# Performance work log

Hardware: AMD Instinct MI355X
Metric: run time of the kernel (lower is better)

The kernel has to match this reference:

```python
import jax, jax.numpy as jnp
import numpy as np

BETA = 1.0

def setup_inputs() -> dict:
    key = jax.random.key(0)
    k1, k2 = jax.random.split(key)
    g = jax.random.normal(k1, (4, 2048, 4096), dtype=jnp.float32)
    W = jax.random.normal(k2, (4096, 16384), dtype=jnp.float32) * 0.02
    return {"g": g, "W": W}

def reference(g, W):
    # column-normalize W over the input dim n (dim=0 in torch)
    norm = jnp.linalg.norm(W, axis=0, keepdims=True)  # [1, n_hidden]
    hidsig = jnp.einsum('btn,nh->bth', g, W / norm)    # [B, T, n_hidden]
    hidlag = (1.0 / BETA) * jax.nn.logsumexp(BETA * hidsig, axis=-1)  # [B, T]
    return hidlag.reshape(-1, hidlag.shape[-1])
```

## Files before the change

kernel.cpp:

```cpp
#include <hip/hip_runtime.h>
#include <hip/hip_bf16.h>

#define M_TOTAL 8192
#define K_DIM   4096
#define H_DIM   16384

#define BM 256
#define BN 256
#define BK 64
#define NKT (K_DIM / BK)

typedef __attribute__((ext_vector_type(8))) short   short8;
typedef __attribute__((ext_vector_type(4))) float   f32x4;
typedef __attribute__((ext_vector_type(8))) unsigned short u16x8;

static __device__ __forceinline__ unsigned short f2bf(float f) {
    unsigned int x = __float_as_uint(f);
    x += 0x7fffu + ((x >> 16) & 1u);
    return (unsigned short)(x >> 16);
}

__global__ void cast_bf16_kernel(const float* __restrict__ in,
                                 unsigned short* __restrict__ out, long n) {
    long i = ((long)blockIdx.x * blockDim.x + threadIdx.x) * 8;
    if (i >= n) return;
    const float4* p = (const float4*)(in + i);
    float4 a = p[0];
    float4 b = p[1];
    u16x8 o;
    o[0] = f2bf(a.x); o[1] = f2bf(a.y); o[2] = f2bf(a.z); o[3] = f2bf(a.w);
    o[4] = f2bf(b.x); o[5] = f2bf(b.y); o[6] = f2bf(b.z); o[7] = f2bf(b.w);
    *(u16x8*)(out + i) = o;
}

__global__ void transpose_norm_kernel(const float* __restrict__ W,
                                      unsigned short* __restrict__ Wt,
                                      float* __restrict__ norm2) {
    __shared__ float tile[64][65];
    __shared__ float np[64];
    const int h0 = blockIdx.x * 64;
    const int n0 = blockIdx.y * 64;
    const int t  = threadIdx.x;
    const int c  = t & 63;
    const int r4 = t >> 6;

    if (t < 64) np[t] = 0.f;
    __syncthreads();

    float sq = 0.f;
#pragma unroll
    for (int it = 0; it < 16; ++it) {
        int r = it * 4 + r4;
        float v = W[(size_t)(n0 + r) * H_DIM + h0 + c];
        tile[r][c] = v;
        sq += v * v;
    }
    atomicAdd(&np[c], sq);
    __syncthreads();

    const int chunk = t & 7;
    const int hr    = t >> 3;
#pragma unroll
    for (int it = 0; it < 2; ++it) {
        int hrow = hr + it * 32;
        u16x8 o;
#pragma unroll
        for (int j = 0; j < 8; ++j)
            o[j] = f2bf(tile[chunk * 8 + j][hrow]);
        *(u16x8*)&Wt[(size_t)(h0 + hrow) * K_DIM + n0 + chunk * 8] = o;
    }
    if (t < 64) atomicAdd(&norm2[h0 + t], np[t]);
}

__global__ __launch_bounds__(512, 2)
void gemm_lse_kernel(const unsigned short* __restrict__ A,
                     const unsigned short* __restrict__ Bt,
                     const float* __restrict__ norm2,
                     float* __restrict__ sums) {
    __shared__ __attribute__((aligned(16))) unsigned short As[2][BM][BK];
    __shared__ __attribute__((aligned(16))) unsigned short Bs[2][BN][BK];

    const int tid  = threadIdx.x;
    const int wave = tid >> 6;
    const int lane = tid & 63;
    const int l15  = lane & 15;
    const int quad = lane >> 4;
    const int wm   = wave >> 2;
    const int wn   = wave & 3;

    const int bid = blockIdx.x;
    const int xcd = bid & 7;
    const int li  = bid >> 3;
    const int m0  = ((xcd & 1) * 16 + (li & 15)) * BM;
    const int h0  = ((xcd >> 1) * 16 + (li >> 4)) * BN;

    const int ri = lane >> 3;
    const int sc = ((lane & 7) ^ ri) * 8;
    const unsigned short* ag = A  + (size_t)(m0 + wave * 8 + ri) * K_DIM + sc;
    const unsigned short* bg = Bt + (size_t)(h0 + wave * 8 + ri) * K_DIM + sc;

#define STAGE_A(BF_, BASE_, KT_)                                               \
    __builtin_amdgcn_global_load_lds(                                          \
        (const __attribute__((address_space(1))) void*)                        \
            (ag + (size_t)(BASE_) * K_DIM + (KT_) * BK),                       \
        (__attribute__((address_space(3))) void*)&As[BF_][(BASE_) + wave * 8][0], \
        16, 0, 0)
#define STAGE_B(BF_, BASE_, KT_)                                               \
    __builtin_amdgcn_global_load_lds(                                          \
        (const __attribute__((address_space(1))) void*)                        \
            (bg + (size_t)(BASE_) * K_DIM + (KT_) * BK),                       \
        (__attribute__((address_space(3))) void*)&Bs[BF_][(BASE_) + wave * 8][0], \
        16, 0, 0)

    const int arow = wm * 128 + l15;
    const int brow = wn * 64 + l15;
    const int sl0  = ((quad)     ^ (l15 & 7)) * 8;
    const int sl1  = ((4 + quad) ^ (l15 & 7)) * 8;

#define LDA(D_, BF_, FM_, KS_) D_ = *(const short8*)&As[BF_][arow + (FM_) * 16][(KS_) ? sl1 : sl0]
#define LDB(D_, BF_, FN_, KS_) D_ = *(const short8*)&Bs[BF_][brow + (FN_) * 16][(KS_) ? sl1 : sl0]

    f32x4 acc[8][4];
#pragma unroll
    for (int i = 0; i < 8; ++i)
#pragma unroll
        for (int j = 0; j < 4; ++j)
            acc[i][j] = (f32x4){0.f, 0.f, 0.f, 0.f};

    short8 sa0[4], sb0[4], sa1[4], sb1[4];

#define CLUSTER(FB_, SA_, SB_)                                                 \
    __builtin_amdgcn_s_barrier();                                              \
    __builtin_amdgcn_s_setprio(1);                                             \
    _Pragma("unroll")                                                          \
    for (int fm = 0; fm < 4; ++fm)                                             \
        _Pragma("unroll")                                                      \
        for (int fn = 0; fn < 4; ++fn)                                         \
            acc[(FB_) + fm][fn] = __builtin_amdgcn_mfma_f32_16x16x32_bf16(     \
                SA_[fm], SB_[fn], acc[(FB_) + fm][fn], 0, 0, 0);               \
    __builtin_amdgcn_s_setprio(0);                                             \
    __builtin_amdgcn_s_barrier()

    STAGE_A(0, 0, 0);   STAGE_A(0, 128, 0);
    STAGE_A(0, 64, 0);  STAGE_A(0, 192, 0);
    STAGE_B(0, 0, 0);   STAGE_B(0, 64, 0);
    STAGE_B(0, 128, 0); STAGE_B(0, 192, 0);
    STAGE_A(1, 0, 1);   STAGE_A(1, 128, 1);
    STAGE_B(1, 0, 1);   STAGE_B(1, 64, 1);
    STAGE_B(1, 128, 1); STAGE_B(1, 192, 1);
    asm volatile("s_waitcnt vmcnt(6)" ::: "memory");
    __builtin_amdgcn_s_barrier();

    LDA(sa0[0], 0, 0, 0); LDA(sa0[1], 0, 1, 0);
    LDA(sa0[2], 0, 2, 0); LDA(sa0[3], 0, 3, 0);
    LDB(sb0[0], 0, 0, 0); LDB(sb0[1], 0, 1, 0);
    LDB(sb0[2], 0, 2, 0); LDB(sb0[3], 0, 3, 0);

#pragma unroll 2
    for (int t = 0; t < NKT; ++t) {
        const int buf  = t & 1;
        const int nbuf = buf ^ 1;

        LDA(sa1[0], buf, 0, 1); LDA(sa1[1], buf, 1, 1);
        LDA(sa1[2], buf, 2, 1); LDA(sa1[3], buf, 3, 1);
        LDB(sb1[0], buf, 0, 1); LDB(sb1[1], buf, 1, 1);
        LDB(sb1[2], buf, 2, 1); LDB(sb1[3], buf, 3, 1);
        if (t < NKT - 1) { STAGE_A(nbuf, 64, t + 1); STAGE_A(nbuf, 192, t + 1); }
        asm volatile("s_waitcnt vmcnt(8)" ::: "memory");
        CLUSTER(0, sa0, sb0);

        LDA(sa0[0], buf, 4, 0); LDA(sa0[1], buf, 5, 0);
        LDA(sa0[2], buf, 6, 0); LDA(sa0[3], buf, 7, 0);
        CLUSTER(0, sa1, sb1);

        LDA(sa1[0], buf, 4, 1); LDA(sa1[1], buf, 5, 1);
        LDA(sa1[2], buf, 6, 1); LDA(sa1[3], buf, 7, 1);
        if (t < NKT - 2) { STAGE_A(buf, 0, t + 2); STAGE_A(buf, 128, t + 2); }
        asm volatile("s_waitcnt vmcnt(4)" ::: "memory");
        CLUSTER(4, sa0, sb0);

        if (t < NKT - 1) {
            LDA(sa0[0], nbuf, 0, 0); LDA(sa0[1], nbuf, 1, 0);
            LDA(sa0[2], nbuf, 2, 0); LDA(sa0[3], nbuf, 3, 0);
            LDB(sb0[0], nbuf, 0, 0); LDB(sb0[1], nbuf, 1, 0);
            LDB(sb0[2], nbuf, 2, 0); LDB(sb0[3], nbuf, 3, 0);
        }
        if (t < NKT - 2) {
            STAGE_B(buf, 0, t + 2);   STAGE_B(buf, 64, t + 2);
            STAGE_B(buf, 128, t + 2); STAGE_B(buf, 192, t + 2);
        }
        CLUSTER(4, sa1, sb1);
    }

    float rn[4];
#pragma unroll
    for (int fn = 0; fn < 4; ++fn)
        rn[fn] = rsqrtf(norm2[h0 + wn * 64 + fn * 16 + l15]);

#pragma unroll
    for (int fm = 0; fm < 8; ++fm) {
#pragma unroll
        for (int r2 = 0; r2 < 4; ++r2) {
            float s = 0.f;
#pragma unroll
            for (int fn = 0; fn < 4; ++fn)
                s += __expf(acc[fm][fn][r2] * rn[fn]);
            s += __shfl_xor(s, 1);
            s += __shfl_xor(s, 2);
            s += __shfl_xor(s, 4);
            s += __shfl_xor(s, 8);
            if (l15 == 0)
                atomicAdd(&sums[m0 + wm * 128 + fm * 16 + quad * 4 + r2], s);
        }
    }
#undef STAGE_A
#undef STAGE_B
#undef LDA
#undef LDB
#undef CLUSTER
}

__global__ void finalize_kernel(const float* __restrict__ sums,
                                float* __restrict__ out, int n) {
    int i = blockIdx.x * blockDim.x + threadIdx.x;
    if (i < n) out[i] = logf(sums[i]);
}

extern "C" void kernel_launch(void* const* d_in, const int* in_sizes, int n_in,
                              void* d_out, int out_size, void* d_ws, size_t ws_size,
                              hipStream_t stream) {
    const float* g = (const float*)d_in[0];
    const float* W = (const float*)d_in[1];
    float* out = (float*)d_out;

    char* ws = (char*)d_ws;
    unsigned short* gbf   = (unsigned short*)ws;
    unsigned short* wt    = (unsigned short*)(ws + (size_t)67108864);
    float*          norm2 = (float*)(ws + (size_t)67108864 + 134217728);
    float*          sums  = (float*)(ws + (size_t)67108864 + 134217728 + 65536);

    hipMemsetAsync(norm2, 0, (H_DIM + M_TOTAL) * sizeof(float), stream);

    cast_bf16_kernel<<<(M_TOTAL * (long)K_DIM) / (256 * 8), 256, 0, stream>>>(
        g, gbf, (long)M_TOTAL * K_DIM);

    transpose_norm_kernel<<<dim3(H_DIM / 64, K_DIM / 64), 256, 0, stream>>>(
        W, wt, norm2);

    gemm_lse_kernel<<<(H_DIM / BN) * (M_TOTAL / BM), 512, 0, stream>>>(
        gbf, wt, norm2, sums);

    finalize_kernel<<<(M_TOTAL + 255) / 256, 256, 0, stream>>>(sums, out, M_TOTAL);
}
```

Before: 1.352 ms.

## Restructure GEMM main loop into two MFMA clusters with single-stage prefetch

Rewrites the K-loop schedule from four interleaved MFMA clusters with partial vmcnt waits and two-tile-ahead global prefetch into two clusters (low and high A halves). Each cluster covers both k-subslices and ends with a full vmcnt(0) wait. Global staging now runs only one tile ahead, and A/B fragment register sets are reorganised to hold both k-steps. This simplifies the dependency tracking and issues larger MFMA bursts, but it shortens the prefetch distance and forces full memory drains each half-iteration, so global load latency may be less hidden.

```diff
diff --git a/kernel.cpp b/kernel.cpp
--- a/kernel.cpp
+++ b/kernel.cpp
@@ -127,69 +127,65 @@
         for (int j = 0; j < 4; ++j)
             acc[i][j] = (f32x4){0.f, 0.f, 0.f, 0.f};
 
-    short8 sa0[4], sb0[4], sa1[4], sb1[4];
-
-#define CLUSTER(FB_, SA_, SB_)                                                 \
+    short8 aL[4][2], aH[4][2], b[4][2];
+
+#define CLUSTER(SA_, FB_)                                                      \
     __builtin_amdgcn_s_barrier();                                              \
     __builtin_amdgcn_s_setprio(1);                                             \
     _Pragma("unroll")                                                          \
-    for (int fm = 0; fm < 4; ++fm)                                             \
+    for (int ks = 0; ks < 2; ++ks)                                             \
         _Pragma("unroll")                                                      \
-        for (int fn = 0; fn < 4; ++fn)                                         \
-            acc[(FB_) + fm][fn] = __builtin_amdgcn_mfma_f32_16x16x32_bf16(     \
-                SA_[fm], SB_[fn], acc[(FB_) + fm][fn], 0, 0, 0);               \
+        for (int fm = 0; fm < 4; ++fm)                                         \
+            _Pragma("unroll")                                                  \
+            for (int fn = 0; fn < 4; ++fn)                                     \
+                acc[(FB_) + fm][fn] = __builtin_amdgcn_mfma_f32_16x16x32_bf16( \
+                    SA_[fm][ks], b[fn][ks], acc[(FB_) + fm][fn], 0, 0, 0);     \
     __builtin_amdgcn_s_setprio(0);                                             \
+    asm volatile("s_waitcnt vmcnt(0)" ::: "memory");                           \
     __builtin_amdgcn_s_barrier()
 
-    STAGE_A(0, 0, 0);   STAGE_A(0, 128, 0);
-    STAGE_A(0, 64, 0);  STAGE_A(0, 192, 0);
+    STAGE_A(0, 0, 0);   STAGE_A(0, 64, 0);
+    STAGE_A(0, 128, 0); STAGE_A(0, 192, 0);
     STAGE_B(0, 0, 0);   STAGE_B(0, 64, 0);
     STAGE_B(0, 128, 0); STAGE_B(0, 192, 0);
-    STAGE_A(1, 0, 1);   STAGE_A(1, 128, 1);
-    STAGE_B(1, 0, 1);   STAGE_B(1, 64, 1);
-    STAGE_B(1, 128, 1); STAGE_B(1, 192, 1);
-    asm volatile("s_waitcnt vmcnt(6)" ::: "memory");
+    asm volatile("s_waitcnt vmcnt(0)" ::: "memory");
     __builtin_amdgcn_s_barrier();
 
-    LDA(sa0[0], 0, 0, 0); LDA(sa0[1], 0, 1, 0);
-    LDA(sa0[2], 0, 2, 0); LDA(sa0[3], 0, 3, 0);
-    LDB(sb0[0], 0, 0, 0); LDB(sb0[1], 0, 1, 0);
-    LDB(sb0[2], 0, 2, 0); LDB(sb0[3], 0, 3, 0);
+    LDA(aL[0][0], 0, 0, 0); LDA(aL[1][0], 0, 1, 0);
+    LDA(aL[2][0], 0, 2, 0); LDA(aL[3][0], 0, 3, 0);
+    LDA(aL[0][1], 0, 0, 1); LDA(aL[1][1], 0, 1, 1);
+    LDA(aL[2][1], 0, 2, 1); LDA(aL[3][1], 0, 3, 1);
 
 #pragma unroll 2
     for (int t = 0; t < NKT; ++t) {
         const int buf  = t & 1;
         const int nbuf = buf ^ 1;
 
-        LDA(sa1[0], buf, 0, 1); LDA(sa1[1], buf, 1, 1);
-        LDA(sa1[2], buf, 2, 1); LDA(sa1[3], buf, 3, 1);
-        LDB(sb1[0], buf, 0, 1); LDB(sb1[1], buf, 1, 1);
-        LDB(sb1[2], buf, 2, 1); LDB(sb1[3], buf, 3, 1);
-        if (t < NKT - 1) { STAGE_A(nbuf, 64, t + 1); STAGE_A(nbuf, 192, t + 1); }
-        asm volatile("s_waitcnt vmcnt(8)" ::: "memory");
-        CLUSTER(0, sa0, sb0);
-
-        LDA(sa0[0], buf, 4, 0); LDA(sa0[1], buf, 5, 0);
-        LDA(sa0[2], buf, 6, 0); LDA(sa0[3], buf, 7, 0);
-        CLUSTER(0, sa1, sb1);
-
-        LDA(sa1[0], buf, 4, 1); LDA(sa1[1], buf, 5, 1);
-        LDA(sa1[2], buf, 6, 1); LDA(sa1[3], buf, 7, 1);
-        if (t < NKT - 2) { STAGE_A(buf, 0, t + 2); STAGE_A(buf, 128, t + 2); }
-        asm volatile("s_waitcnt vmcnt(4)" ::: "memory");
-        CLUSTER(4, sa0, sb0);
-
         if (t < NKT - 1) {
-            LDA(sa0[0], nbuf, 0, 0); LDA(sa0[1], nbuf, 1, 0);
-            LDA(sa0[2], nbuf, 2, 0); LDA(sa0[3], nbuf, 3, 0);
-            LDB(sb0[0], nbuf, 0, 0); LDB(sb0[1], nbuf, 1, 0);
-            LDB(sb0[2], nbuf, 2, 0); LDB(sb0[3], nbuf, 3, 0);
+            STAGE_A(nbuf, 0, t + 1);   STAGE_A(nbuf, 64, t + 1);
+            STAGE_A(nbuf, 128, t + 1); STAGE_A(nbuf, 192, t + 1);
         }
-        if (t < NKT - 2) {
-            STAGE_B(buf, 0, t + 2);   STAGE_B(buf, 64, t + 2);
-            STAGE_B(buf, 128, t + 2); STAGE_B(buf, 192, t + 2);
+        LDB(b[0][0], buf, 0, 0); LDB(b[1][0], buf, 1, 0);
+        LDB(b[2][0], buf, 2, 0); LDB(b[3][0], buf, 3, 0);
+        LDB(b[0][1], buf, 0, 1); LDB(b[1][1], buf, 1, 1);
+        LDB(b[2][1], buf, 2, 1); LDB(b[3][1], buf, 3, 1);
+        LDA(aH[0][0], buf, 4, 0); LDA(aH[1][0], buf, 5, 0);
+        LDA(aH[2][0], buf, 6, 0); LDA(aH[3][0], buf, 7, 0);
+        LDA(aH[0][1], buf, 4, 1); LDA(aH[1][1], buf, 5, 1);
+        LDA(aH[2][1], buf, 6, 1); LDA(aH[3][1], buf, 7, 1);
+
+        CLUSTER(aL, 0);
+
+        if (t < NKT - 1) {
+            STAGE_B(nbuf, 0, t + 1);   STAGE_B(nbuf, 64, t + 1);
+            STAGE_B(nbuf, 128, t + 1); STAGE_B(nbuf, 192, t + 1);
+            LDA(aL[0][0], nbuf, 0, 0); LDA(aL[1][0], nbuf, 1, 0);
+            LDA(aL[2][0], nbuf, 2, 0); LDA(aL[3][0], nbuf, 3, 0);
+            LDA(aL[0][1], nbuf, 0, 1); LDA(aL[1][1], nbuf, 1, 1);
+            LDA(aL[2][1], nbuf, 2, 1); LDA(aL[3][1], nbuf, 3, 1);
         }
-        CLUSTER(4, sa1, sb1);
+
+        CLUSTER(aH, 4);
     }
 
     float rn[4];
```

Result: slower. 1.560 ms (+15.4%).

## Reschedule GEMM main loop with one barrier per MFMA cluster and earlier staging

Applied to the files above, without the earlier changes.

Restructures the double-buffered bf16 MFMA main loop so each of the four MFMA clusters is preceded by a single barrier plus a priority raise, instead of a barrier before and after every cluster. Global-to-LDS stage loads are issued right after the barrier, ahead of the LDS fragment reads, and the vmcnt waits move to the loop top and before the B staging, with separate counts for the last iterations. The goal is to halve the barrier count and overlap global loads with MFMA work better. The new wait counts must still guard every LDS buffer reuse, and a miscount could create a race.

```diff
diff --git a/kernel.cpp b/kernel.cpp
--- a/kernel.cpp
+++ b/kernel.cpp
@@ -129,17 +129,13 @@
 
     short8 sa0[4], sb0[4], sa1[4], sb1[4];
 
-#define CLUSTER(FB_, SA_, SB_)                                                 \
-    __builtin_amdgcn_s_barrier();                                              \
-    __builtin_amdgcn_s_setprio(1);                                             \
+#define MFMA16(FB_, SA_, SB_)                                                  \
     _Pragma("unroll")                                                          \
     for (int fm = 0; fm < 4; ++fm)                                             \
         _Pragma("unroll")                                                      \
         for (int fn = 0; fn < 4; ++fn)                                         \
             acc[(FB_) + fm][fn] = __builtin_amdgcn_mfma_f32_16x16x32_bf16(     \
-                SA_[fm], SB_[fn], acc[(FB_) + fm][fn], 0, 0, 0);               \
-    __builtin_amdgcn_s_setprio(0);                                             \
-    __builtin_amdgcn_s_barrier()
+                SA_[fm], SB_[fn], acc[(FB_) + fm][fn], 0, 0, 0)
 
     STAGE_A(0, 0, 0);   STAGE_A(0, 128, 0);
     STAGE_A(0, 64, 0);  STAGE_A(0, 192, 0);
@@ -161,35 +157,49 @@
         const int buf  = t & 1;
         const int nbuf = buf ^ 1;
 
+        if (t < NKT - 1) { asm volatile("s_waitcnt vmcnt(6)" ::: "memory"); }
+        else             { asm volatile("s_waitcnt vmcnt(0)" ::: "memory"); }
+        __builtin_amdgcn_s_barrier();
+        __builtin_amdgcn_s_setprio(1);
+        if (t < NKT - 1) { STAGE_A(nbuf, 64, t + 1); STAGE_A(nbuf, 192, t + 1); }
         LDA(sa1[0], buf, 0, 1); LDA(sa1[1], buf, 1, 1);
         LDA(sa1[2], buf, 2, 1); LDA(sa1[3], buf, 3, 1);
         LDB(sb1[0], buf, 0, 1); LDB(sb1[1], buf, 1, 1);
         LDB(sb1[2], buf, 2, 1); LDB(sb1[3], buf, 3, 1);
-        if (t < NKT - 1) { STAGE_A(nbuf, 64, t + 1); STAGE_A(nbuf, 192, t + 1); }
-        asm volatile("s_waitcnt vmcnt(8)" ::: "memory");
-        CLUSTER(0, sa0, sb0);
-
+        MFMA16(0, sa0, sb0);
+        __builtin_amdgcn_s_setprio(0);
+
+        __builtin_amdgcn_s_barrier();
+        __builtin_amdgcn_s_setprio(1);
         LDA(sa0[0], buf, 4, 0); LDA(sa0[1], buf, 5, 0);
         LDA(sa0[2], buf, 6, 0); LDA(sa0[3], buf, 7, 0);
-        CLUSTER(0, sa1, sb1);
-
+        MFMA16(0, sa1, sb1);
+        __builtin_amdgcn_s_setprio(0);
+
+        __builtin_amdgcn_s_barrier();
+        __builtin_amdgcn_s_setprio(1);
+        if (t < NKT - 2) { STAGE_A(buf, 0, t + 2); STAGE_A(buf, 128, t + 2); }
         LDA(sa1[0], buf, 4, 1); LDA(sa1[1], buf, 5, 1);
         LDA(sa1[2], buf, 6, 1); LDA(sa1[3], buf, 7, 1);
-        if (t < NKT - 2) { STAGE_A(buf, 0, t + 2); STAGE_A(buf, 128, t + 2); }
-        asm volatile("s_waitcnt vmcnt(4)" ::: "memory");
-        CLUSTER(4, sa0, sb0);
-
+        MFMA16(4, sa0, sb0);
+        __builtin_amdgcn_s_setprio(0);
+
+        if (t < NKT - 2) { asm volatile("s_waitcnt vmcnt(4)" ::: "memory"); }
+        else             { asm volatile("s_waitcnt vmcnt(2)" ::: "memory"); }
+        __builtin_amdgcn_s_barrier();
+        __builtin_amdgcn_s_setprio(1);
+        if (t < NKT - 2) {
+            STAGE_B(buf, 0, t + 2);   STAGE_B(buf, 64, t + 2);
+            STAGE_B(buf, 128, t + 2); STAGE_B(buf, 192, t + 2);
+        }
         if (t < NKT - 1) {
             LDA(sa0[0], nbuf, 0, 0); LDA(sa0[1], nbuf, 1, 0);
             LDA(sa0[2], nbuf, 2, 0); LDA(sa0[3], nbuf, 3, 0);
             LDB(sb0[0], nbuf, 0, 0); LDB(sb0[1], nbuf, 1, 0);
             LDB(sb0[2], nbuf, 2, 0); LDB(sb0[3], nbuf, 3, 0);
         }
-        if (t < NKT - 2) {
-            STAGE_B(buf, 0, t + 2);   STAGE_B(buf, 64, t + 2);
-            STAGE_B(buf, 128, t + 2); STAGE_B(buf, 192, t + 2);
-        }
-        CLUSTER(4, sa1, sb1);
+        MFMA16(4, sa1, sb1);
+        __builtin_amdgcn_s_setprio(0);
     }
 
     float rn[4];
@@ -217,7 +227,7 @@
 #undef STAGE_B
 #undef LDA
 #undef LDB
-#undef CLUSTER
+#undef MFMA16
 }
 
 __global__ void finalize_kernel(const float* __restrict__ sums,
```

Measured after the change: 1.496 ms. 1.11x slower.

## Switch GEMM inner tiles from 16x16x32 to 32x32x16 bf16 MFMA

Applied to the files above, without the earlier changes.

Replaces the 16x16x32 MFMA fragments with 32x32x16 MFMA fragments. This changes the LDS fragment loads, the accumulator layout (4x2 f32x16 tiles) and the epilogue row mapping used for the exp-sum reduction. The larger MFMA shape is meant to cut LDS read traffic per FLOP and the instruction count. The waitcnt ordering is also adjusted, with vmcnt(0) on the final iterations. In exchange, the row-index mapping and the wider shuffle reduction add correctness risk.

```diff
diff --git a/kernel.cpp b/kernel.cpp
--- a/kernel.cpp
+++ b/kernel.cpp
@@ -10,9 +10,10 @@
 #define BK 64
 #define NKT (K_DIM / BK)
 
-typedef __attribute__((ext_vector_type(8))) short   short8;
-typedef __attribute__((ext_vector_type(4))) float   f32x4;
-typedef __attribute__((ext_vector_type(8))) unsigned short u16x8;
+typedef __attribute__((ext_vector_type(8)))  short  short8;
+typedef __attribute__((ext_vector_type(4)))  float  f32x4;
+typedef __attribute__((ext_vector_type(16))) float  f32x16;
+typedef __attribute__((ext_vector_type(8)))  unsigned short u16x8;
 
 static __device__ __forceinline__ unsigned short f2bf(float f) {
     unsigned int x = __float_as_uint(f);
@@ -83,8 +84,9 @@
     const int tid  = threadIdx.x;
     const int wave = tid >> 6;
     const int lane = tid & 63;
-    const int l15  = lane & 15;
-    const int quad = lane >> 4;
+    const int l31  = lane & 31;
+    const int l7   = lane & 7;
+    const int hi32 = lane >> 5;
     const int wm   = wave >> 2;
     const int wn   = wave & 3;
 
@@ -95,7 +97,7 @@
     const int h0  = ((xcd >> 1) * 16 + (li >> 4)) * BN;
 
     const int ri = lane >> 3;
-    const int sc = ((lane & 7) ^ ri) * 8;
+    const int sc = (l7 ^ ri) * 8;
     const unsigned short* ag = A  + (size_t)(m0 + wave * 8 + ri) * K_DIM + sc;
     const unsigned short* bg = Bt + (size_t)(h0 + wave * 8 + ri) * K_DIM + sc;
 
@@ -112,32 +114,35 @@
         (__attribute__((address_space(3))) void*)&Bs[BF_][(BASE_) + wave * 8][0], \
         16, 0, 0)
 
-    const int arow = wm * 128 + l15;
-    const int brow = wn * 64 + l15;
-    const int sl0  = ((quad)     ^ (l15 & 7)) * 8;
-    const int sl1  = ((4 + quad) ^ (l15 & 7)) * 8;
-
-#define LDA(D_, BF_, FM_, KS_) D_ = *(const short8*)&As[BF_][arow + (FM_) * 16][(KS_) ? sl1 : sl0]
-#define LDB(D_, BF_, FN_, KS_) D_ = *(const short8*)&Bs[BF_][brow + (FN_) * 16][(KS_) ? sl1 : sl0]
-
-    f32x4 acc[8][4];
-#pragma unroll
-    for (int i = 0; i < 8; ++i)
-#pragma unroll
-        for (int j = 0; j < 4; ++j)
-            acc[i][j] = (f32x4){0.f, 0.f, 0.f, 0.f};
-
-    short8 sa0[4], sb0[4], sa1[4], sb1[4];
+#define LDA32(D_, BF_, FM_, KF_)                                               \
+    D_ = *(const short8*)&As[BF_][wm * 128 + (FM_) * 32 + l31]                 \
+                             [(((KF_) * 2 + hi32) ^ l7) * 8]
+#define LDB32(D_, BF_, FN_, KF_)                                               \
+    D_ = *(const short8*)&Bs[BF_][wn * 64 + (FN_) * 32 + l31]                  \
+                             [(((KF_) * 2 + hi32) ^ l7) * 8]
+
+    f32x16 acc[4][2];
+#pragma unroll
+    for (int i = 0; i < 4; ++i)
+#pragma unroll
+        for (int j = 0; j < 2; ++j)
+#pragma unroll
+            for (int r = 0; r < 16; ++r)
+                acc[i][j][r] = 0.f;
+
+    short8 sa0[2][2], sb0[2][2], sa1[2][2], sb1[2][2];
 
 #define CLUSTER(FB_, SA_, SB_)                                                 \
     __builtin_amdgcn_s_barrier();                                              \
     __builtin_amdgcn_s_setprio(1);                                             \
     _Pragma("unroll")                                                          \
-    for (int fm = 0; fm < 4; ++fm)                                             \
+    for (int kk = 0; kk < 2; ++kk)                                             \
         _Pragma("unroll")                                                      \
-        for (int fn = 0; fn < 4; ++fn)                                         \
-            acc[(FB_) + fm][fn] = __builtin_amdgcn_mfma_f32_16x16x32_bf16(     \
-                SA_[fm], SB_[fn], acc[(FB_) + fm][fn], 0, 0, 0);               \
+        for (int fm = 0; fm < 2; ++fm)                                         \
+            _Pragma("unroll")                                                  \
+            for (int fn = 0; fn < 2; ++fn)                                     \
+                acc[(FB_) + fm][fn] = __builtin_amdgcn_mfma_f32_32x32x16_bf16( \
+                    SA_[fm][kk], SB_[fn][kk], acc[(FB_) + fm][fn], 0, 0, 0);   \
     __builtin_amdgcn_s_setprio(0);                                             \
     __builtin_amdgcn_s_barrier()
 
@@ -151,72 +156,73 @@
     asm volatile("s_waitcnt vmcnt(6)" ::: "memory");
     __builtin_amdgcn_s_barrier();
 
-    LDA(sa0[0], 0, 0, 0); LDA(sa0[1], 0, 1, 0);
-    LDA(sa0[2], 0, 2, 0); LDA(sa0[3], 0, 3, 0);
-    LDB(sb0[0], 0, 0, 0); LDB(sb0[1], 0, 1, 0);
-    LDB(sb0[2], 0, 2, 0); LDB(sb0[3], 0, 3, 0);
+    LDA32(sa0[0][0], 0, 0, 0); LDA32(sa0[0][1], 0, 0, 1);
+    LDA32(sa0[1][0], 0, 1, 0); LDA32(sa0[1][1], 0, 1, 1);
+    LDB32(sb0[0][0], 0, 0, 0); LDB32(sb0[0][1], 0, 0, 1);
+    LDB32(sb0[1][0], 0, 1, 0); LDB32(sb0[1][1], 0, 1, 1);
 
 #pragma unroll 2
     for (int t = 0; t < NKT; ++t) {
         const int buf  = t & 1;
         const int nbuf = buf ^ 1;
 
-        LDA(sa1[0], buf, 0, 1); LDA(sa1[1], buf, 1, 1);
-        LDA(sa1[2], buf, 2, 1); LDA(sa1[3], buf, 3, 1);
-        LDB(sb1[0], buf, 0, 1); LDB(sb1[1], buf, 1, 1);
-        LDB(sb1[2], buf, 2, 1); LDB(sb1[3], buf, 3, 1);
         if (t < NKT - 1) { STAGE_A(nbuf, 64, t + 1); STAGE_A(nbuf, 192, t + 1); }
-        asm volatile("s_waitcnt vmcnt(8)" ::: "memory");
+        LDA32(sa1[0][0], buf, 0, 2); LDA32(sa1[0][1], buf, 0, 3);
+        LDA32(sa1[1][0], buf, 1, 2); LDA32(sa1[1][1], buf, 1, 3);
+        LDB32(sb1[0][0], buf, 0, 2); LDB32(sb1[0][1], buf, 0, 3);
+        LDB32(sb1[1][0], buf, 1, 2); LDB32(sb1[1][1], buf, 1, 3);
+        if (t < NKT - 1) { asm volatile("s_waitcnt vmcnt(8)" ::: "memory"); }
+        else             { asm volatile("s_waitcnt vmcnt(0)" ::: "memory"); }
         CLUSTER(0, sa0, sb0);
 
-        LDA(sa0[0], buf, 4, 0); LDA(sa0[1], buf, 5, 0);
-        LDA(sa0[2], buf, 6, 0); LDA(sa0[3], buf, 7, 0);
+        LDA32(sa0[0][0], buf, 2, 0); LDA32(sa0[0][1], buf, 2, 1);
+        LDA32(sa0[1][0], buf, 3, 0); LDA32(sa0[1][1], buf, 3, 1);
         CLUSTER(0, sa1, sb1);
 
-        LDA(sa1[0], buf, 4, 1); LDA(sa1[1], buf, 5, 1);
-        LDA(sa1[2], buf, 6, 1); LDA(sa1[3], buf, 7, 1);
         if (t < NKT - 2) { STAGE_A(buf, 0, t + 2); STAGE_A(buf, 128, t + 2); }
-        asm volatile("s_waitcnt vmcnt(4)" ::: "memory");
-        CLUSTER(4, sa0, sb0);
-
-        if (t < NKT - 1) {
-            LDA(sa0[0], nbuf, 0, 0); LDA(sa0[1], nbuf, 1, 0);
-            LDA(sa0[2], nbuf, 2, 0); LDA(sa0[3], nbuf, 3, 0);
-            LDB(sb0[0], nbuf, 0, 0); LDB(sb0[1], nbuf, 1, 0);
-            LDB(sb0[2], nbuf, 2, 0); LDB(sb0[3], nbuf, 3, 0);
-        }
+        LDA32(sa1[0][0], buf, 2, 2); LDA32(sa1[0][1], buf, 2, 3);
+        LDA32(sa1[1][0], buf, 3, 2); LDA32(sa1[1][1], buf, 3, 3);
+        if (t < NKT - 2) { asm volatile("s_waitcnt vmcnt(4)" ::: "memory"); }
+        else             { asm volatile("s_waitcnt vmcnt(0)" ::: "memory"); }
+        CLUSTER(2, sa0, sb0);
+
         if (t < NKT - 2) {
             STAGE_B(buf, 0, t + 2);   STAGE_B(buf, 64, t + 2);
             STAGE_B(buf, 128, t + 2); STAGE_B(buf, 192, t + 2);
         }
-        CLUSTER(4, sa1, sb1);
-    }
-
-    float rn[4];
-#pragma unroll
-    for (int fn = 0; fn < 4; ++fn)
-        rn[fn] = rsqrtf(norm2[h0 + wn * 64 + fn * 16 + l15]);
-
-#pragma unroll
-    for (int fm = 0; fm < 8; ++fm) {
-#pragma unroll
-        for (int r2 = 0; r2 < 4; ++r2) {
-            float s = 0.f;
-#pragma unroll
-            for (int fn = 0; fn < 4; ++fn)
-                s += __expf(acc[fm][fn][r2] * rn[fn]);
+        if (t < NKT - 1) {
+            LDA32(sa0[0][0], nbuf, 0, 0); LDA32(sa0[0][1], nbuf, 0, 1);
+            LDA32(sa0[1][0], nbuf, 1, 0); LDA32(sa0[1][1], nbuf, 1, 1);
+            LDB32(sb0[0][0], nbuf, 0, 0); LDB32(sb0[0][1], nbuf, 0, 1);
+            LDB32(sb0[1][0], nbuf, 1, 0); LDB32(sb0[1][1], nbuf, 1, 1);
+        }
+        CLUSTER(2, sa1, sb1);
+    }
+
+    float rn2[2];
+#pragma unroll
+    for (int fn = 0; fn < 2; ++fn)
+        rn2[fn] = rsqrtf(norm2[h0 + wn * 64 + fn * 32 + l31]);
+
+#pragma unroll
+    for (int i = 0; i < 4; ++i) {
+#pragma unroll
+        for (int r = 0; r < 16; ++r) {
+            float s = __expf(acc[i][0][r] * rn2[0]) + __expf(acc[i][1][r] * rn2[1]);
             s += __shfl_xor(s, 1);
             s += __shfl_xor(s, 2);
             s += __shfl_xor(s, 4);
             s += __shfl_xor(s, 8);
-            if (l15 == 0)
-                atomicAdd(&sums[m0 + wm * 128 + fm * 16 + quad * 4 + r2], s);
+            s += __shfl_xor(s, 16);
+            if (l31 == 0)
+                atomicAdd(&sums[m0 + wm * 128 + i * 32 +
+                                (r & 3) + 8 * (r >> 2) + 4 * hi32], s);
         }
     }
 #undef STAGE_A
 #undef STAGE_B
-#undef LDA
-#undef LDB
+#undef LDA32
+#undef LDB32
 #undef CLUSTER
 }
 
```

After: 1.699 ms. 25.6% more time.
